# Performance work log

Hardware: AMD Instinct MI355X
Metric: run time of the kernel (lower is better)

## Reference

```python
import jax, jax.numpy as jnp
import numpy as np

TWO_PI = 2.0 * np.pi

def diff_round(x):
    # smooth differentiable rounding used throughout the repo
    return x - jnp.sin(TWO_PI * x) / TWO_PI

def harder_diff_round(x):
    return diff_round(diff_round(diff_round(x)))

def differentiable_eq(a, b):
    a = harder_diff_round(a)
    b = harder_diff_round(b)
    return harder_diff_round(a * b + (1.0 - a) * (1.0 - b))

def differentiable_and(a, b):
    return diff_round(a) * diff_round(b)

def filter_mask_of_interest(mask, initial_mask_id):
    # mask: [B, N, dx, dy, 4]; initial_mask_id: [B, N, 4]
    c = differentiable_eq(mask, initial_mask_id[:, :, None, None, :])  # [B,N,dx,dy,4]
    a = differentiable_and(c[..., 0], c[..., 1])
    b = differentiable_and(c[..., 2], c[..., 3])
    return differentiable_and(a, b)  # [B, N, dx, dy]

def get_out_image(mask_combined, initial_mask_id, resized_image):
    m = filter_mask_of_interest(mask_combined, initial_mask_id)[..., None]  # [B,N,dx,dy,1]
    masked = m * resized_image
    # per-area masked mean over (dx, dy, channel)
    num = jnp.sum(masked, axis=(2, 3, 4))           # [B, N]
    den = jnp.sum(m, axis=(2, 3, 4))                # [B, N]
    mean = num / den
    return m * mean[:, :, None, None, None]

def setup_inputs() -> dict:
    key = jax.random.key(0)
    k1, k2, k3, k4, k5 = jax.random.split(key, 5)
    B, N, DX, DY = 2, 8192, 16, 16
    return {
        "resized_image": jax.random.uniform(k1, (B, N, DX, DY, 1), jnp.float32),
        "mask_combined": jax.random.uniform(k2, (B, N, DX, DY, 4), jnp.float32),
        "mask_combined_alt": jax.random.uniform(k3, (B, N, DX, DY, 4), jnp.float32),
        "initial_mask_id": jax.random.uniform(k4, (B, N, 4), jnp.float32),
        "mask_new_bi_channel": jax.random.uniform(k5, (B, N, DX, DY, 2), jnp.float32),
        "mask_index": 0,
    }

def reference(resized_image, mask_combined, mask_combined_alt, initial_mask_id, mask_new_bi_channel, mask_index):
    # batched_v_Apply_on_single_area: nested vmap over (batch, area), vectorized here
    out_image = get_out_image(mask_combined, initial_mask_id, resized_image)
    out_image_alt = get_out_image(mask_combined_alt, initial_mask_id, resized_image)
    return (out_image, out_image_alt)
```

## Files before the change

kernel.cpp:

```cpp
#include <hip/hip_runtime.h>

#define INV_2PI 0.15915494309189535f

__device__ __forceinline__ float vsin_pinned(float x) {
    float r;
    asm volatile("v_sin_f32 %0, %1" : "=v"(r) : "v"(x));
    return r;
}

template <int N>
__device__ __forceinline__ void dround_batch(float* c) {
    float s[N];
#pragma unroll
    for (int i = 0; i < N; ++i) s[i] = vsin_pinned(c[i]);
#pragma unroll
    for (int i = 0; i < N; ++i) c[i] = __builtin_fmaf(-INV_2PI, s[i], c[i]);
}

__device__ __forceinline__ void filter_tail(float* c, const float* hb,
                                            const float* vb, float* m) {
#pragma unroll
    for (int i = 0; i < 16; ++i) {
        float om = 1.0f - c[i];
        c[i] = __builtin_fmaf(c[i], hb[i & 3], om * vb[i & 3]);
    }
    dround_batch<16>(c); dround_batch<16>(c); dround_batch<16>(c);
    dround_batch<16>(c);
    float p[8];
#pragma unroll
    for (int j = 0; j < 4; ++j) {
        p[2 * j]     = c[4 * j]     * c[4 * j + 1];
        p[2 * j + 1] = c[4 * j + 2] * c[4 * j + 3];
    }
    dround_batch<8>(p);
#pragma unroll
    for (int j = 0; j < 4; ++j) m[j] = p[2 * j] * p[2 * j + 1];
}

__global__ __launch_bounds__(256) void De_conv_areas_kernel(
    const float* __restrict__ img,
    const float* __restrict__ mask,
    const float* __restrict__ mask_alt,
    const float* __restrict__ mask_id,
    float* __restrict__ out,
    float* __restrict__ out_alt,
    int n_areas)
{
    const int lane = threadIdx.x & 63;
    int area = blockIdx.x * (blockDim.x >> 6) + (threadIdx.x >> 6);
    if (area >= n_areas) return;
    area = __builtin_amdgcn_readfirstlane(area);

    const size_t base = (size_t)area * 256;

    const float4* mp = (const float4*)mask     + base + lane;
    const float4* ap = (const float4*)mask_alt + base + lane;
    const float*  ip = img + base + lane;

    float4 q0 = mp[0], q1 = mp[64], q2 = mp[128], q3 = mp[192];
    float4 a0 = ap[0], a1 = ap[64], a2 = ap[128], a3 = ap[192];
    float  i0 = ip[0], i1 = ip[64], i2 = ip[128], i3 = ip[192];
    float4 idv = *(const float4*)(mask_id + (size_t)area * 4);

    float c0[20] = { idv.x, idv.y, idv.z, idv.w,
                     q0.x, q0.y, q0.z, q0.w,  q1.x, q1.y, q1.z, q1.w,
                     q2.x, q2.y, q2.z, q2.w,  q3.x, q3.y, q3.z, q3.w };
    dround_batch<20>(c0); dround_batch<20>(c0); dround_batch<20>(c0);

    float hb[4] = { c0[0], c0[1], c0[2], c0[3] };
    float vb[4];
#pragma unroll
    for (int k = 0; k < 4; ++k) vb[k] = 1.0f - hb[k];

    float m0[4];
    filter_tail(c0 + 4, hb, vb, m0);

    float c1[16] = { a0.x, a0.y, a0.z, a0.w,  a1.x, a1.y, a1.z, a1.w,
                     a2.x, a2.y, a2.z, a2.w,  a3.x, a3.y, a3.z, a3.w };
    dround_batch<16>(c1); dround_batch<16>(c1); dround_batch<16>(c1);
    float m1[4];
    filter_tail(c1, hb, vb, m1);

    float im[4] = { i0, i1, i2, i3 };
    float sm0 = 0.f, si0 = 0.f, sm1 = 0.f, si1 = 0.f;
#pragma unroll
    for (int j = 0; j < 4; ++j) {
        sm0 += m0[j]; si0 += m0[j] * im[j];
        sm1 += m1[j]; si1 += m1[j] * im[j];
    }
#pragma unroll
    for (int off = 32; off; off >>= 1) {
        sm0 += __shfl_xor(sm0, off, 64);
        si0 += __shfl_xor(si0, off, 64);
        sm1 += __shfl_xor(sm1, off, 64);
        si1 += __shfl_xor(si1, off, 64);
    }

    const float mean0 = (sm0 > 0.f) ? (si0 / sm0) : 0.f;
    const float mean1 = (sm1 > 0.f) ? (si1 / sm1) : 0.f;

    float* d0 = out     + base + lane;
    float* d1 = out_alt + base + lane;
#pragma unroll
    for (int k = 0; k < 4; ++k) {
        d0[64 * k] = m0[k] * mean0;
        d1[64 * k] = m1[k] * mean1;
    }
}

extern "C" void kernel_launch(void* const* d_in, const int* in_sizes, int n_in,
                              void* d_out, int out_size, void* d_ws, size_t ws_size,
                              hipStream_t stream) {
    const float* img      = (const float*)d_in[0];
    const float* mask     = (const float*)d_in[1];
    const float* mask_alt = (const float*)d_in[2];
    const float* mask_id  = (const float*)d_in[3];

    const int n_areas = out_size / 512;
    float* out     = (float*)d_out;
    float* out_alt = out + (size_t)n_areas * 256;

    const int waves_per_block = 4;
    const int blocks = (n_areas + waves_per_block - 1) / waves_per_block;
    De_conv_areas_kernel<<<blocks, 256, 0, stream>>>(
        img, mask, mask_alt, mask_id, out, out_alt, n_areas);
}
```

Measured before the change: 196.2 us.

## Make waves persistent over several areas with double-buffered register prefetch

Each wave now handles four areas with a grid stride. The loads for the next area go into a second register buffer while the sin-heavy compute for the current area runs, and sched_barrier keeps the compiler from moving them together. The goal is to hide global memory latency behind the transcendental math. The cost is roughly double the register footprint per wave, which can lower occupancy, and fewer waves in the grid.

```diff
diff --git a/kernel.cpp b/kernel.cpp
--- a/kernel.cpp
+++ b/kernel.cpp
@@ -37,34 +37,39 @@
     for (int j = 0; j < 4; ++j) m[j] = p[2 * j] * p[2 * j + 1];
 }
 
-__global__ __launch_bounds__(256) void De_conv_areas_kernel(
-    const float* __restrict__ img,
-    const float* __restrict__ mask,
-    const float* __restrict__ mask_alt,
-    const float* __restrict__ mask_id,
-    float* __restrict__ out,
-    float* __restrict__ out_alt,
-    int n_areas)
-{
-    const int lane = threadIdx.x & 63;
-    int area = blockIdx.x * (blockDim.x >> 6) + (threadIdx.x >> 6);
-    if (area >= n_areas) return;
+struct AreaBuf {
+    float4 q0, q1, q2, q3;
+    float4 a0, a1, a2, a3;
+    float  i0, i1, i2, i3;
+    float4 idv;
+};
+
+__device__ __forceinline__ void load_area(AreaBuf& b,
+        const float* __restrict__ img, const float4* __restrict__ mask4,
+        const float4* __restrict__ alt4, const float* __restrict__ mask_id,
+        int area, int lane) {
     area = __builtin_amdgcn_readfirstlane(area);
+    const size_t base = (size_t)area * 256;
+    const float4* mp = mask4 + base + lane;
+    b.q0 = mp[0]; b.q1 = mp[64]; b.q2 = mp[128]; b.q3 = mp[192];
+    const float4* ap = alt4 + base + lane;
+    b.a0 = ap[0]; b.a1 = ap[64]; b.a2 = ap[128]; b.a3 = ap[192];
+    const float* ip = img + base + lane;
+    b.i0 = ip[0]; b.i1 = ip[64]; b.i2 = ip[128]; b.i3 = ip[192];
+    b.idv = *(const float4*)(mask_id + (size_t)area * 4);
+}
 
+__device__ __forceinline__ void compute_store(const AreaBuf& b,
+        float* __restrict__ out, float* __restrict__ out_alt,
+        int area, int lane) {
+    area = __builtin_amdgcn_readfirstlane(area);
     const size_t base = (size_t)area * 256;
 
-    const float4* mp = (const float4*)mask     + base + lane;
-    const float4* ap = (const float4*)mask_alt + base + lane;
-    const float*  ip = img + base + lane;
-
-    float4 q0 = mp[0], q1 = mp[64], q2 = mp[128], q3 = mp[192];
-    float4 a0 = ap[0], a1 = ap[64], a2 = ap[128], a3 = ap[192];
-    float  i0 = ip[0], i1 = ip[64], i2 = ip[128], i3 = ip[192];
-    float4 idv = *(const float4*)(mask_id + (size_t)area * 4);
-
-    float c0[20] = { idv.x, idv.y, idv.z, idv.w,
-                     q0.x, q0.y, q0.z, q0.w,  q1.x, q1.y, q1.z, q1.w,
-                     q2.x, q2.y, q2.z, q2.w,  q3.x, q3.y, q3.z, q3.w };
+    float c0[20] = { b.idv.x, b.idv.y, b.idv.z, b.idv.w,
+                     b.q0.x, b.q0.y, b.q0.z, b.q0.w,
+                     b.q1.x, b.q1.y, b.q1.z, b.q1.w,
+                     b.q2.x, b.q2.y, b.q2.z, b.q2.w,
+                     b.q3.x, b.q3.y, b.q3.z, b.q3.w };
     dround_batch<20>(c0); dround_batch<20>(c0); dround_batch<20>(c0);
 
     float hb[4] = { c0[0], c0[1], c0[2], c0[3] };
@@ -75,13 +80,15 @@
     float m0[4];
     filter_tail(c0 + 4, hb, vb, m0);
 
-    float c1[16] = { a0.x, a0.y, a0.z, a0.w,  a1.x, a1.y, a1.z, a1.w,
-                     a2.x, a2.y, a2.z, a2.w,  a3.x, a3.y, a3.z, a3.w };
+    float c1[16] = { b.a0.x, b.a0.y, b.a0.z, b.a0.w,
+                     b.a1.x, b.a1.y, b.a1.z, b.a1.w,
+                     b.a2.x, b.a2.y, b.a2.z, b.a2.w,
+                     b.a3.x, b.a3.y, b.a3.z, b.a3.w };
     dround_batch<16>(c1); dround_batch<16>(c1); dround_batch<16>(c1);
     float m1[4];
     filter_tail(c1, hb, vb, m1);
 
-    float im[4] = { i0, i1, i2, i3 };
+    float im[4] = { b.i0, b.i1, b.i2, b.i3 };
     float sm0 = 0.f, si0 = 0.f, sm1 = 0.f, si1 = 0.f;
 #pragma unroll
     for (int j = 0; j < 4; ++j) {
@@ -108,6 +115,42 @@
     }
 }
 
+__global__ __launch_bounds__(256) void De_conv_areas_kernel(
+    const float* __restrict__ img,
+    const float* __restrict__ mask,
+    const float* __restrict__ mask_alt,
+    const float* __restrict__ mask_id,
+    float* __restrict__ out,
+    float* __restrict__ out_alt,
+    int n_areas, int n_waves)
+{
+    const int lane = threadIdx.x & 63;
+    const int w = blockIdx.x * (blockDim.x >> 6) + (threadIdx.x >> 6);
+    if (w >= n_areas) return;
+
+    const float4* mask4 = (const float4*)mask;
+    const float4* alt4  = (const float4*)mask_alt;
+
+    AreaBuf A, B;
+    int tA = w;
+    int tB = w + n_waves;
+    load_area(A, img, mask4, alt4, mask_id, tA, lane);
+
+    for (;;) {
+        if (tB < n_areas) load_area(B, img, mask4, alt4, mask_id, tB, lane);
+        __builtin_amdgcn_sched_barrier(0);
+        compute_store(A, out, out_alt, tA, lane);
+        if (tB >= n_areas) break;
+
+        tA = tB + n_waves;
+        if (tA < n_areas) load_area(A, img, mask4, alt4, mask_id, tA, lane);
+        __builtin_amdgcn_sched_barrier(0);
+        compute_store(B, out, out_alt, tB, lane);
+        if (tA >= n_areas) break;
+        tB = tA + n_waves;
+    }
+}
+
 extern "C" void kernel_launch(void* const* d_in, const int* in_sizes, int n_in,
                               void* d_out, int out_size, void* d_ws, size_t ws_size,
                               hipStream_t stream) {
@@ -120,8 +163,10 @@
     float* out     = (float*)d_out;
     float* out_alt = out + (size_t)n_areas * 256;
 
+    const int areas_per_wave = 4;
+    const int n_waves = (n_areas + areas_per_wave - 1) / areas_per_wave;
     const int waves_per_block = 4;
-    const int blocks = (n_areas + waves_per_block - 1) / waves_per_block;
+    const int blocks = (n_waves + waves_per_block - 1) / waves_per_block;
     De_conv_areas_kernel<<<blocks, 256, 0, stream>>>(
-        img, mask, mask_alt, mask_id, out, out_alt, n_areas);
+        img, mask, mask_alt, mask_id, out, out_alt, n_areas, n_waves);
 }
```

Result: no change. 198.7 us (+1.3%).

## Use persistent waves with double-buffered async global-to-LDS mask staging

Applied to the files above, without the earlier changes.

Converts the one-wave-per-area kernel into a persistent kernel of 2048 waves. Each wave walks a contiguous run of areas and prefetches the next area's two masks straight into LDS with global_load_lds, double-buffered, while the current area is computed. Manual vmcnt waits order the stages, and block IDs are remapped in an XCD-aware way. The aim is to overlap memory latency with the sine-heavy compute, at the cost of far fewer resident waves per CU and fragile hand-counted waitcnt synchronisation.

```diff
diff --git a/kernel.cpp b/kernel.cpp
--- a/kernel.cpp
+++ b/kernel.cpp
@@ -37,32 +37,57 @@
     for (int j = 0; j < 4; ++j) m[j] = p[2 * j] * p[2 * j + 1];
 }
 
-__global__ __launch_bounds__(256) void De_conv_areas_kernel(
-    const float* __restrict__ img,
-    const float* __restrict__ mask,
-    const float* __restrict__ mask_alt,
-    const float* __restrict__ mask_id,
-    float* __restrict__ out,
-    float* __restrict__ out_alt,
-    int n_areas)
+struct SideRegs { float i0, i1, i2, i3; float4 idv; };
+
+#define WAIT12() asm volatile("s_waitcnt vmcnt(12)" ::: "memory")
+#define WAIT0()  asm volatile("s_waitcnt vmcnt(0)"  ::: "memory")
+
+typedef __attribute__((address_space(1))) const void gvoid_t;
+typedef __attribute__((address_space(3))) void svoid_t;
+
+__device__ __forceinline__ void stage_area(
+        float* sslot, SideRegs& r,
+        const float* __restrict__ img, const float* __restrict__ mask,
+        const float* __restrict__ mask_alt, const float* __restrict__ mask_id,
+        int area, int lane)
 {
-    const int lane = threadIdx.x & 63;
-    int area = blockIdx.x * (blockDim.x >> 6) + (threadIdx.x >> 6);
-    if (area >= n_areas) return;
     area = __builtin_amdgcn_readfirstlane(area);
+    const float* gm = mask     + (size_t)area * 1024 + lane * 4;
+    const float* ga = mask_alt + (size_t)area * 1024 + lane * 4;
+#pragma unroll
+    for (int i = 0; i < 4; ++i)
+        __builtin_amdgcn_global_load_lds((gvoid_t*)(gm + i * 256),
+                                         (svoid_t*)(sslot + i * 256),
+                                         16, 0, 0);
+#pragma unroll
+    for (int i = 0; i < 4; ++i)
+        __builtin_amdgcn_global_load_lds((gvoid_t*)(ga + i * 256),
+                                         (svoid_t*)(sslot + 1024 + i * 256),
+                                         16, 0, 0);
+    const float* ip = img + (size_t)area * 256 + lane;
+    r.i0 = ip[0]; r.i1 = ip[64]; r.i2 = ip[128]; r.i3 = ip[192];
+    r.idv = *(const float4*)(mask_id + (size_t)area * 4);
+}
 
+__device__ __forceinline__ void compute_store(
+        const float* sslot, const SideRegs& r,
+        float* __restrict__ out, float* __restrict__ out_alt,
+        int area, int lane)
+{
+    area = __builtin_amdgcn_readfirstlane(area);
     const size_t base = (size_t)area * 256;
 
-    const float4* mp = (const float4*)mask     + base + lane;
-    const float4* ap = (const float4*)mask_alt + base + lane;
-    const float*  ip = img + base + lane;
+    const float* sm = sslot + lane * 4;
+    float4 q0 = *(const float4*)(sm);
+    float4 q1 = *(const float4*)(sm + 256);
+    float4 q2 = *(const float4*)(sm + 512);
+    float4 q3 = *(const float4*)(sm + 768);
+    float4 a0 = *(const float4*)(sm + 1024);
+    float4 a1 = *(const float4*)(sm + 1280);
+    float4 a2 = *(const float4*)(sm + 1536);
+    float4 a3 = *(const float4*)(sm + 1792);
 
-    float4 q0 = mp[0], q1 = mp[64], q2 = mp[128], q3 = mp[192];
-    float4 a0 = ap[0], a1 = ap[64], a2 = ap[128], a3 = ap[192];
-    float  i0 = ip[0], i1 = ip[64], i2 = ip[128], i3 = ip[192];
-    float4 idv = *(const float4*)(mask_id + (size_t)area * 4);
-
-    float c0[20] = { idv.x, idv.y, idv.z, idv.w,
+    float c0[20] = { r.idv.x, r.idv.y, r.idv.z, r.idv.w,
                      q0.x, q0.y, q0.z, q0.w,  q1.x, q1.y, q1.z, q1.w,
                      q2.x, q2.y, q2.z, q2.w,  q3.x, q3.y, q3.z, q3.w };
     dround_batch<20>(c0); dround_batch<20>(c0); dround_batch<20>(c0);
@@ -81,7 +106,7 @@
     float m1[4];
     filter_tail(c1, hb, vb, m1);
 
-    float im[4] = { i0, i1, i2, i3 };
+    float im[4] = { r.i0, r.i1, r.i2, r.i3 };
     float sm0 = 0.f, si0 = 0.f, sm1 = 0.f, si1 = 0.f;
 #pragma unroll
     for (int j = 0; j < 4; ++j) {
@@ -108,6 +133,50 @@
     }
 }
 
+__global__ __launch_bounds__(256) void De_conv_areas_kernel(
+    const float* __restrict__ img,
+    const float* __restrict__ mask,
+    const float* __restrict__ mask_alt,
+    const float* __restrict__ mask_id,
+    float* __restrict__ out,
+    float* __restrict__ out_alt,
+    int n_areas, int apw)
+{
+    __shared__ __align__(16) float lds[4][2][2048];
+
+    const int lane = threadIdx.x & 63;
+    const int wv   = threadIdx.x >> 6;
+
+    int bid = blockIdx.x;
+    int sbid = (gridDim.x % 8 == 0)
+             ? ((bid & 7) * (gridDim.x >> 3) + (bid >> 3)) : bid;
+
+    const int w  = sbid * 4 + wv;
+    const int a0 = w * apw;
+    if (a0 >= n_areas) return;
+    const int end = (a0 + apw < n_areas) ? (a0 + apw) : n_areas;
+
+    float* slotA = &lds[wv][0][0];
+    float* slotB = &lds[wv][1][0];
+    SideRegs rA, rB;
+
+    stage_area(slotA, rA, img, mask, mask_alt, mask_id, a0, lane);
+
+    for (int t = a0;; t += 2) {
+        const bool n1 = (t + 1 < end);
+        if (n1) { stage_area(slotB, rB, img, mask, mask_alt, mask_id, t + 1, lane); WAIT12(); }
+        else    { WAIT0(); }
+        compute_store(slotA, rA, out, out_alt, t, lane);
+        if (!n1) break;
+
+        const bool n2 = (t + 2 < end);
+        if (n2) { stage_area(slotA, rA, img, mask, mask_alt, mask_id, t + 2, lane); WAIT12(); }
+        else    { WAIT0(); }
+        compute_store(slotB, rB, out, out_alt, t + 1, lane);
+        if (!n2) break;
+    }
+}
+
 extern "C" void kernel_launch(void* const* d_in, const int* in_sizes, int n_in,
                               void* d_out, int out_size, void* d_ws, size_t ws_size,
                               hipStream_t stream) {
@@ -120,8 +189,9 @@
     float* out     = (float*)d_out;
     float* out_alt = out + (size_t)n_areas * 256;
 
-    const int waves_per_block = 4;
-    const int blocks = (n_areas + waves_per_block - 1) / waves_per_block;
+    const int n_waves = 2048;
+    const int apw = (n_areas + n_waves - 1) / n_waves;
+    const int blocks = 512;
     De_conv_areas_kernel<<<blocks, 256, 0, stream>>>(
-        img, mask, mask_alt, mask_id, out, out_alt, n_areas);
+        img, mask, mask_alt, mask_id, out, out_alt, n_areas, apw);
 }
```

Result: slower. 204.0 us (+4.0%).
